# Optimization experiments

Measured on AMD Instinct MI355X. Metric: run time of the kernel, lower is better.

The kernel has to match this reference:

```python
import jax, jax.numpy as jnp
import numpy as np

TAU = 0.5


def _l2norm(x):
    # F.normalize(p=2, dim=1): x / max(||x||, eps) with eps=1e-12
    n = jnp.sqrt(jnp.sum(x * x, axis=1, keepdims=True))
    return x / jnp.maximum(n, 1e-12)


def setup_inputs() -> dict:
    key = jax.random.key(0)
    k1, k2 = jax.random.split(key)
    N, D = 8192, 512
    left = jax.random.normal(k1, (N, D), dtype=jnp.float32)
    right = jax.random.normal(k2, (N, D), dtype=jnp.float32)
    return {"left": left, "right": right}


def reference(left, right) -> jnp.ndarray:
    zl = _l2norm(left)
    zr = _l2norm(right)
    # [N, N] cosine-similarity matrices
    refl_sim = jnp.exp(jnp.matmul(zl, zl.T) / TAU)
    between_sim = jnp.exp(jnp.matmul(zl, zr.T) / TAU)
    between_diag = jnp.diagonal(between_sim)
    refl_diag = jnp.diagonal(refl_sim)
    denom = refl_sim.sum(axis=1) + between_sim.sum(axis=1) - refl_diag
    loss = -jnp.log(between_diag / denom)  # [N]
    return loss
```

## Files before the change

### kernel.cpp

```cpp
#include <hip/hip_runtime.h>

#define NROWS 8192
#define DDIM 512
#define ZROWS 16384
#define BM 256
#define BN 256
#define BK 64
#define KTILES (DDIM / BK)
#define NLL 32
#define NLR_BLOCKS 1024
#define NSYM_BLOCKS 528
#define NBLOCKS (NLR_BLOCKS + NSYM_BLOCKS)

typedef __attribute__((ext_vector_type(8))) short short8;
typedef __attribute__((ext_vector_type(4))) float f32x4;

__device__ __forceinline__ unsigned short f2bf(float f) {
  unsigned int u = __float_as_uint(f);
  u = (u + 0x7FFFu + ((u >> 16) & 1u)) >> 16;
  return (unsigned short)u;
}

__global__ __launch_bounds__(256) void nrm_kernel(const float* __restrict__ left,
                                                  const float* __restrict__ right,
                                                  unsigned short* __restrict__ Z,
                                                  float* __restrict__ dlr) {
  const int i = blockIdx.x;
  const int t = threadIdx.x;
  const float2 lv = ((const float2*)(left + (size_t)i * DDIM))[t];
  const float2 rv = ((const float2*)(right + (size_t)i * DDIM))[t];
  float ssl = lv.x * lv.x + lv.y * lv.y;
  float ssr = rv.x * rv.x + rv.y * rv.y;
  float slr = lv.x * rv.x + lv.y * rv.y;
#pragma unroll
  for (int m = 1; m < 64; m <<= 1) {
    ssl += __shfl_xor(ssl, m);
    ssr += __shfl_xor(ssr, m);
    slr += __shfl_xor(slr, m);
  }
  __shared__ float red[3][4];
  const int w = t >> 6;
  if ((t & 63) == 0) { red[0][w] = ssl; red[1][w] = ssr; red[2][w] = slr; }
  __syncthreads();
  ssl = red[0][0] + red[0][1] + red[0][2] + red[0][3];
  ssr = red[1][0] + red[1][1] + red[1][2] + red[1][3];
  slr = red[2][0] + red[2][1] + red[2][2] + red[2][3];
  const float invl = 1.0f / fmaxf(sqrtf(ssl), 1e-12f);
  const float invr = 1.0f / fmaxf(sqrtf(ssr), 1e-12f);
  if (t == 0) dlr[i] = slr * invl * invr;
  ushort2 zl2; zl2.x = f2bf(lv.x * invl); zl2.y = f2bf(lv.y * invl);
  ushort2 zr2; zr2.x = f2bf(rv.x * invr); zr2.y = f2bf(rv.y * invr);
  ((ushort2*)(Z + (size_t)i * DDIM))[t] = zl2;
  ((ushort2*)(Z + (size_t)(NROWS + i) * DDIM))[t] = zr2;
}

__global__ __launch_bounds__(512) void sim_kernel(const unsigned short* __restrict__ Z,
                                                  float* __restrict__ partial) {
  __shared__ __align__(16) unsigned short sA[2][BM * BK];
  __shared__ __align__(16) unsigned short sB[2][BN * BK];

  int tm, tn; bool sym = false;
  {
    const int bid = blockIdx.x;
    if (bid < NLR_BLOCKS) {
      tm = bid >> 5; tn = 32 + (bid & 31);
    } else {
      const int b2 = bid - NLR_BLOCKS;
      int i = (int)(32.5f - sqrtf(32.5f * 32.5f - 2.0f * (float)b2));
      if (i < 0) i = 0; if (i > 31) i = 31;
      while (i > 0 && (32 * i - i * (i - 1) / 2) > b2) --i;
      while (i < 31 && (32 * (i + 1) - (i + 1) * i / 2) <= b2) ++i;
      tm = i; tn = i + (b2 - (32 * i - i * (i - 1) / 2));
      sym = (tn != tm);
    }
  }

  const int t = threadIdx.x;
  const int l = t & 63;
  const int w = t >> 6;
  const int wm = w >> 2;
  const int wn = w & 3;
  const int lr = l & 15;
  const int lk = l >> 4;

  f32x4 acc[8][4];
#pragma unroll
  for (int a = 0; a < 8; ++a)
#pragma unroll
    for (int b = 0; b < 4; ++b)
#pragma unroll
      for (int r = 0; r < 4; ++r) acc[a][b][r] = 0.0f;

  const unsigned short* Abase = Z + (size_t)tm * BM * DDIM;
  const unsigned short* Bbase = Z + (size_t)tn * BN * DDIM;

  const int srow = t >> 3;
  const int scol = ((t & 7) ^ (srow & 7)) * 8;

#define STAGE_A(bufi, k0)                                                         \
  {                                                                               \
    _Pragma("unroll")                                                             \
    for (int j = 0; j < 4; ++j) {                                                 \
      __builtin_amdgcn_global_load_lds(                                           \
          (const __attribute__((address_space(1))) void*)(Abase +                 \
              (size_t)(j * 64 + srow) * DDIM + (k0) + scol),                      \
          (__attribute__((address_space(3))) void*)(&sA[bufi][(j * 512 + t) * 8]),\
          16, 0, 0);                                                              \
    }                                                                             \
  }
#define STAGE_B(bufi, k0)                                                         \
  {                                                                               \
    _Pragma("unroll")                                                             \
    for (int j = 0; j < 4; ++j) {                                                 \
      __builtin_amdgcn_global_load_lds(                                           \
          (const __attribute__((address_space(1))) void*)(Bbase +                 \
              (size_t)(j * 64 + srow) * DDIM + (k0) + scol),                      \
          (__attribute__((address_space(3))) void*)(&sB[bufi][(j * 512 + t) * 8]),\
          16, 0, 0);                                                              \
    }                                                                             \
  }

  STAGE_A(0, 0);
  STAGE_B(0, 0);
  asm volatile("s_waitcnt vmcnt(0)" ::: "memory");
  __builtin_amdgcn_s_barrier();
  __builtin_amdgcn_sched_barrier(0);

  short8 af[4][2], ag[4][2], bf[4][2];

#define DS_A(dst, fmb)                                                             \
  _Pragma("unroll")                                                                \
  for (int fm = 0; fm < 4; ++fm)                                                   \
    _Pragma("unroll")                                                              \
    for (int ks = 0; ks < 2; ++ks) {                                               \
      const int row = wm * 128 + ((fmb) + fm) * 16 + lr;                           \
      dst[fm][ks] = *(const short8*)&sA[cur][row * BK + ((ks * 4 + lk) ^ (lr & 7)) * 8]; \
    }

#define DS_B2(fnb)                                                                 \
  _Pragma("unroll")                                                                \
  for (int fn = 0; fn < 2; ++fn)                                                   \
    _Pragma("unroll")                                                              \
    for (int ks = 0; ks < 2; ++ks) {                                               \
      const int row = wn * 64 + ((fnb) + fn) * 16 + lr;                            \
      bf[(fnb) + fn][ks] = *(const short8*)&sB[cur][row * BK + ((ks * 4 + lk) ^ (lr & 7)) * 8]; \
    }

#define MFMA16(A, fmb, fnb)                                                        \
  __builtin_amdgcn_s_setprio(1);                                                   \
  _Pragma("unroll")                                                                \
  for (int fm = 0; fm < 4; ++fm)                                                   \
    _Pragma("unroll")                                                              \
    for (int fn = 0; fn < 2; ++fn)                                                 \
      _Pragma("unroll")                                                            \
      for (int ks = 0; ks < 2; ++ks)                                               \
        acc[(fmb) + fm][(fnb) + fn] =                                              \
            __builtin_amdgcn_mfma_f32_16x16x32_bf16(A[fm][ks], bf[(fnb) + fn][ks], \
                                                    acc[(fmb) + fm][(fnb) + fn],   \
                                                    0, 0, 0);                      \
  __builtin_amdgcn_s_setprio(0);

#define SBAR __builtin_amdgcn_sched_barrier(0)
#define BAR  __builtin_amdgcn_s_barrier()

#pragma unroll
  for (int kt = 0; kt < KTILES; ++kt) {
    const int cur = kt & 1;
    const int nxt = cur ^ 1;
    DS_A(af, 0); DS_B2(0);
    if (kt + 1 < KTILES) STAGE_A(nxt, (kt + 1) * BK);
    SBAR; BAR; SBAR;
    MFMA16(af, 0, 0);
    SBAR; BAR; SBAR;
    DS_B2(2);
    if (kt + 1 < KTILES) STAGE_B(nxt, (kt + 1) * BK);
    SBAR; BAR; SBAR;
    MFMA16(af, 0, 2);
    SBAR; BAR; SBAR;
    DS_A(ag, 4);
    SBAR; BAR; SBAR;
    MFMA16(ag, 4, 0);
    SBAR; BAR; SBAR;
    asm volatile("s_waitcnt vmcnt(0)" ::: "memory");
    SBAR; BAR; SBAR;
    MFMA16(ag, 4, 2);
    SBAR; BAR; SBAR;
  }

  float* rsum = (float*)&sA[0][0];
  float* csum = rsum + BM;
  if (t < BM) { rsum[t] = 0.0f; csum[t] = 0.0f; }
  __syncthreads();
  float c0 = 0.0f, c1 = 0.0f, c2 = 0.0f, c3 = 0.0f;
#pragma unroll
  for (int fm = 0; fm < 8; ++fm) {
#pragma unroll
    for (int r = 0; r < 4; ++r) {
      float e0 = __expf(2.0f * acc[fm][0][r]);
      float e1 = __expf(2.0f * acc[fm][1][r]);
      float e2 = __expf(2.0f * acc[fm][2][r]);
      float e3 = __expf(2.0f * acc[fm][3][r]);
      float v = e0 + e1 + e2 + e3;
      v += __shfl_xor(v, 1);
      v += __shfl_xor(v, 2);
      v += __shfl_xor(v, 4);
      v += __shfl_xor(v, 8);
      if (lr == 0) atomicAdd(&rsum[wm * 128 + fm * 16 + lk * 4 + r], v);
      c0 += e0; c1 += e1; c2 += e2; c3 += e3;
    }
  }
  if (sym) {
    c0 += __shfl_xor(c0, 16); c0 += __shfl_xor(c0, 32);
    c1 += __shfl_xor(c1, 16); c1 += __shfl_xor(c1, 32);
    c2 += __shfl_xor(c2, 16); c2 += __shfl_xor(c2, 32);
    c3 += __shfl_xor(c3, 16); c3 += __shfl_xor(c3, 32);
    if (l < 16) {
      atomicAdd(&csum[wn * 64 +  0 + lr], c0);
      atomicAdd(&csum[wn * 64 + 16 + lr], c1);
      atomicAdd(&csum[wn * 64 + 32 + lr], c2);
      atomicAdd(&csum[wn * 64 + 48 + lr], c3);
    }
  }
  __syncthreads();
  if (t < BM) partial[(size_t)tn * NROWS + tm * BM + t] = rsum[t];
  if (sym && t < BM) partial[(size_t)tm * NROWS + tn * BM + t] = csum[t];
}

__global__ __launch_bounds__(256) void fin_kernel(const float* __restrict__ partial,
                                                  const float* __restrict__ dlr,
                                                  float* __restrict__ out) {
  const int i = blockIdx.x * 256 + threadIdx.x;
  float s = 0.0f;
#pragma unroll 8
  for (int p = 0; p < 64; ++p) s += partial[(size_t)p * NROWS + i];
  out[i] = logf(s - 7.38905609893065f) - 2.0f * dlr[i];
}

extern "C" void kernel_launch(void* const* d_in, const int* in_sizes, int n_in,
                              void* d_out, int out_size, void* d_ws, size_t ws_size,
                              hipStream_t stream) {
  const float* left = (const float*)d_in[0];
  const float* right = (const float*)d_in[1];
  float* out = (float*)d_out;

  unsigned short* Z = (unsigned short*)d_ws;
  char* p = (char*)d_ws + (size_t)ZROWS * DDIM * 2;
  float* dlr = (float*)p;
  float* partial = (float*)(p + (size_t)NROWS * 4);

  nrm_kernel<<<NROWS, 256, 0, stream>>>(left, right, Z, dlr);
  sim_kernel<<<NBLOCKS, 512, 0, stream>>>(Z, partial);
  fin_kernel<<<NROWS / 256, 256, 0, stream>>>(partial, dlr, out);
}
```

Baseline: 158.4 us.

## Interleave global-to-LDS prefetch in quarter chunks across MFMA phases with partial vmcnt waits

Restructures the double-buffered K loop into an unrolled pair of tiles. Global-to-LDS loads are split into half-tile chunks issued in different MFMA phases, so next-tile data is staged more finely and the previous buffer's portions are refilled as soon as they are consumed. Waits use vmcnt(6) instead of draining all loads, and explicit lgkmcnt(0) waits are added before each MFMA group. The goal is better overlap of memory traffic with compute, at the cost of more complex buffer-hazard reasoning.

```diff
diff --git a/kernel.cpp b/kernel.cpp
--- a/kernel.cpp
+++ b/kernel.cpp
@@ -7,7 +7,6 @@
 #define BN 256
 #define BK 64
 #define KTILES (DDIM / BK)
-#define NLL 32
 #define NLR_BLOCKS 1024
 #define NSYM_BLOCKS 528
 #define NBLOCKS (NLR_BLOCKS + NSYM_BLOCKS)
@@ -97,53 +96,41 @@
   const int srow = t >> 3;
   const int scol = ((t & 7) ^ (srow & 7)) * 8;
 
-#define STAGE_A(bufi, k0)                                                         \
-  {                                                                               \
-    _Pragma("unroll")                                                             \
-    for (int j = 0; j < 4; ++j) {                                                 \
-      __builtin_amdgcn_global_load_lds(                                           \
-          (const __attribute__((address_space(1))) void*)(Abase +                 \
-              (size_t)(j * 64 + srow) * DDIM + (k0) + scol),                      \
-          (__attribute__((address_space(3))) void*)(&sA[bufi][(j * 512 + t) * 8]),\
-          16, 0, 0);                                                              \
-    }                                                                             \
-  }
-#define STAGE_B(bufi, k0)                                                         \
-  {                                                                               \
-    _Pragma("unroll")                                                             \
-    for (int j = 0; j < 4; ++j) {                                                 \
-      __builtin_amdgcn_global_load_lds(                                           \
-          (const __attribute__((address_space(1))) void*)(Bbase +                 \
-              (size_t)(j * 64 + srow) * DDIM + (k0) + scol),                      \
-          (__attribute__((address_space(3))) void*)(&sB[bufi][(j * 512 + t) * 8]),\
-          16, 0, 0);                                                              \
-    }                                                                             \
-  }
-
-  STAGE_A(0, 0);
-  STAGE_B(0, 0);
-  asm volatile("s_waitcnt vmcnt(0)" ::: "memory");
-  __builtin_amdgcn_s_barrier();
-  __builtin_amdgcn_sched_barrier(0);
+#define STAGE_AJ(bufi, k0, j)                                                     \
+  __builtin_amdgcn_global_load_lds(                                               \
+      (const __attribute__((address_space(1))) void*)(Abase +                     \
+          (size_t)((j) * 64 + srow) * DDIM + (k0) + scol),                        \
+      (__attribute__((address_space(3))) void*)(&sA[bufi][((j) * 512 + t) * 8]),  \
+      16, 0, 0);
+#define STAGE_BJ(bufi, k0, j)                                                     \
+  __builtin_amdgcn_global_load_lds(                                               \
+      (const __attribute__((address_space(1))) void*)(Bbase +                     \
+          (size_t)((j) * 64 + srow) * DDIM + (k0) + scol),                        \
+      (__attribute__((address_space(3))) void*)(&sB[bufi][((j) * 512 + t) * 8]),  \
+      16, 0, 0);
+#define STAGE_A02(b, k0) { STAGE_AJ(b, k0, 0) STAGE_AJ(b, k0, 2) }
+#define STAGE_A13(b, k0) { STAGE_AJ(b, k0, 1) STAGE_AJ(b, k0, 3) }
+#define STAGE_B01(b, k0) { STAGE_BJ(b, k0, 0) STAGE_BJ(b, k0, 1) }
+#define STAGE_B23(b, k0) { STAGE_BJ(b, k0, 2) STAGE_BJ(b, k0, 3) }
 
   short8 af[4][2], ag[4][2], bf[4][2];
 
-#define DS_A(dst, fmb)                                                             \
+#define DS_A(dst, bufi, fmb)                                                       \
   _Pragma("unroll")                                                                \
   for (int fm = 0; fm < 4; ++fm)                                                   \
     _Pragma("unroll")                                                              \
     for (int ks = 0; ks < 2; ++ks) {                                               \
       const int row = wm * 128 + ((fmb) + fm) * 16 + lr;                           \
-      dst[fm][ks] = *(const short8*)&sA[cur][row * BK + ((ks * 4 + lk) ^ (lr & 7)) * 8]; \
-    }
-
-#define DS_B2(fnb)                                                                 \
+      dst[fm][ks] = *(const short8*)&sA[bufi][row * BK + ((ks * 4 + lk) ^ (lr & 7)) * 8]; \
+    }
+
+#define DS_B2(bufi, fnb)                                                           \
   _Pragma("unroll")                                                                \
   for (int fn = 0; fn < 2; ++fn)                                                   \
     _Pragma("unroll")                                                              \
     for (int ks = 0; ks < 2; ++ks) {                                               \
       const int row = wn * 64 + ((fnb) + fn) * 16 + lr;                            \
-      bf[(fnb) + fn][ks] = *(const short8*)&sB[cur][row * BK + ((ks * 4 + lk) ^ (lr & 7)) * 8]; \
+      bf[(fnb) + fn][ks] = *(const short8*)&sB[bufi][row * BK + ((ks * 4 + lk) ^ (lr & 7)) * 8]; \
     }
 
 #define MFMA16(A, fmb, fnb)                                                        \
@@ -160,28 +147,55 @@
                                                     0, 0, 0);                      \
   __builtin_amdgcn_s_setprio(0);
 
-#define SBAR __builtin_amdgcn_sched_barrier(0)
-#define BAR  __builtin_amdgcn_s_barrier()
-
-#pragma unroll
-  for (int kt = 0; kt < KTILES; ++kt) {
-    const int cur = kt & 1;
-    const int nxt = cur ^ 1;
-    DS_A(af, 0); DS_B2(0);
-    if (kt + 1 < KTILES) STAGE_A(nxt, (kt + 1) * BK);
-    SBAR; BAR; SBAR;
+#define SBAR  __builtin_amdgcn_sched_barrier(0)
+#define BAR   __builtin_amdgcn_s_barrier()
+#define LGKM0 { asm volatile("s_waitcnt lgkmcnt(0)" ::: "memory"); SBAR; }
+#define VM6   asm volatile("s_waitcnt vmcnt(6)" ::: "memory")
+#define VM0   asm volatile("s_waitcnt vmcnt(0)" ::: "memory")
+
+  STAGE_A02(0, 0); STAGE_A13(0, 0); STAGE_B01(0, 0); STAGE_B23(0, 0);
+  STAGE_A02(1, BK); STAGE_B01(1, BK); STAGE_B23(1, BK);
+  VM6;
+  BAR; SBAR;
+
+#pragma unroll
+  for (int it = 0; it < 4; ++it) {
+    const int kt = 2 * it;
+    DS_A(af, 0, 0); DS_B2(0, 0);
+    STAGE_A13(1, (kt + 1) * BK);
+    SBAR; BAR; LGKM0;
     MFMA16(af, 0, 0);
     SBAR; BAR; SBAR;
-    DS_B2(2);
-    if (kt + 1 < KTILES) STAGE_B(nxt, (kt + 1) * BK);
-    SBAR; BAR; SBAR;
+    DS_B2(0, 2);
+    if (kt + 2 < KTILES) STAGE_A02(0, (kt + 2) * BK);
+    SBAR; BAR; LGKM0;
     MFMA16(af, 0, 2);
     SBAR; BAR; SBAR;
-    DS_A(ag, 4);
-    SBAR; BAR; SBAR;
+    DS_A(ag, 0, 4);
+    if (kt + 2 < KTILES) STAGE_B01(0, (kt + 2) * BK);
+    SBAR; BAR; LGKM0;
     MFMA16(ag, 4, 0);
     SBAR; BAR; SBAR;
-    asm volatile("s_waitcnt vmcnt(0)" ::: "memory");
+    if (kt + 2 < KTILES) { STAGE_B23(0, (kt + 2) * BK); VM6; } else { VM0; }
+    SBAR; BAR; SBAR;
+    MFMA16(ag, 4, 2);
+    SBAR; BAR; SBAR;
+    DS_A(af, 1, 0); DS_B2(1, 0);
+    if (kt + 2 < KTILES) STAGE_A13(0, (kt + 2) * BK);
+    SBAR; BAR; LGKM0;
+    MFMA16(af, 0, 0);
+    SBAR; BAR; SBAR;
+    DS_B2(1, 2);
+    if (kt + 3 < KTILES) STAGE_A02(1, (kt + 3) * BK);
+    SBAR; BAR; LGKM0;
+    MFMA16(af, 0, 2);
+    SBAR; BAR; SBAR;
+    DS_A(ag, 1, 4);
+    if (kt + 3 < KTILES) STAGE_B01(1, (kt + 3) * BK);
+    SBAR; BAR; LGKM0;
+    MFMA16(ag, 4, 0);
+    SBAR; BAR; SBAR;
+    if (kt + 3 < KTILES) { STAGE_B23(1, (kt + 3) * BK); VM6; } else { VM0; }
     SBAR; BAR; SBAR;
     MFMA16(ag, 4, 2);
     SBAR; BAR; SBAR;
```

Result: no change. 161.5 us (+2.0%).
